# Kernel optimization log

Hardware: AMD Instinct MI355X
Metric: run time of the kernel (lower is better)

Reference implementation:

```python
import jax, jax.numpy as jnp
import numpy as np

TAU_CONVERGE = 0.01
N_STABLE = 2
B, L, DIM = 8, 4096, 1024
H, M = 16, 64
D_HEAD = DIM // H


def setup_inputs() -> dict:
    key = jax.random.key(0)
    k1, k2, k3, k4, k5, k6 = jax.random.split(key, 6)
    z_current = jax.random.normal(k1, (B, L, DIM), dtype=jnp.float32)
    # small perturbation so per-head velocity straddles tau_converge
    z_prev = z_current + 0.00125 * jax.random.normal(k2, (B, L, DIM), dtype=jnp.float32)
    codebook = jax.random.normal(k3, (H, M, D_HEAD), dtype=jnp.float32) * 0.02
    frozen_values = jax.random.normal(k4, (B, L, H, D_HEAD), dtype=jnp.float32)
    consecutive_converged = jax.random.randint(k5, (B, L, H), 0, 2, dtype=jnp.int32)
    crystallised = jax.random.randint(k6, (B, L, H), 0, 2) > 0
    return {
        "z_current": z_current,
        "z_prev": z_prev,
        "codebook": codebook,
        "frozen_values": frozen_values,
        "consecutive_converged": consecutive_converged,
        "crystallised": crystallised,
    }


def reference(z_current, z_prev, codebook, frozen_values, consecutive_converged, crystallised):
    """One crystallisation step: velocity -> counters -> snap-to-codebook -> enforce.

    Mirrors ConvergenceMonitor.update_and_crystallise followed by enforce(),
    with MultiHeadedCodebook.quantise(hard=True) for the codebook snap.
    All freeze/snap logic is outside the gradient graph (torch.no_grad/detach).
    """
    sg = jax.lax.stop_gradient
    zc = z_current.reshape(B, L, H, D_HEAD)   # [B,L,H,d]
    zp = z_prev.reshape(B, L, H, D_HEAD)

    # per-head velocity norm (detached in original)
    velocity = jnp.linalg.norm(sg(zc) - sg(zp), axis=-1)       # [B,L,H]
    converged = velocity < TAU_CONVERGE
    cc_new = jnp.where(converged, consecutive_converged + 1, 0)
    newly = (cc_new >= N_STABLE) & (~crystallised)             # [B,L,H] bool

    # hard nearest-neighbour quantise per head (no_grad in original)
    z_sg = sg(zc)
    cb = sg(codebook)
    # squared L2 distance: ||z||^2 - 2 z.c + ||c||^2  -> [B,L,H,M]
    d2 = (jnp.sum(z_sg * z_sg, axis=-1, keepdims=True)
          - 2.0 * jnp.einsum('blhd,hmd->blhm', z_sg, cb)
          + jnp.sum(cb * cb, axis=-1)[None, None])
    idx = jnp.argmin(d2, axis=-1)                              # [B,L,H]
    # gather nearest entries per head: codebook[h, idx[b,l,h]] -> [B,L,H,d]
    entries = cb[jnp.arange(H)[None, None, :], idx]

    # masked scatter of newly crystallised heads into frozen values
    frozen_new = jnp.where(newly[..., None], entries, sg(frozen_values))
    crystal_new = crystallised | newly

    # enforce: overwrite crystallised heads with frozen codebook values
    z_enforced = jnp.where(crystal_new[..., None], frozen_new, zc).reshape(B, L, DIM)
    return z_enforced, crystal_new, newly, cc_new, frozen_new
```

## Files before the change

### kernel.cpp

```cpp
#include <hip/hip_runtime.h>

#define BB 8
#define LL 4096
#define DIM 1024
#define HH 16
#define MM 64
#define DH 64

constexpr long long NZ = (long long)BB * LL * DIM;
constexpr long long NG = (long long)BB * LL * HH;
constexpr long long O_Z   = 0;
constexpr long long O_CRY = NZ;
constexpr long long O_NEW = NZ + NG;
constexpr long long O_CC  = NZ + 2 * NG;
constexpr long long O_FR  = NZ + 3 * NG;


#define ROWS 8

__global__ __launch_bounds__(256) void crystal_main(
    const float4* __restrict__ zc4,
    const float4* __restrict__ zp4,
    const float4* __restrict__ fr4,
    const int*    __restrict__ ccount,
    const int*    __restrict__ cryst,
    unsigned int* __restrict__ masks,
    float* __restrict__ out)
{
    __shared__ float lds_cry[ROWS * HH];
    __shared__ float lds_new[ROWS * HH];
    __shared__ float lds_cc [ROWS * HH];

    const int t   = threadIdx.x;
    const int h   = t >> 4;
    const int sub = t & 15;

    const long long row0 = (long long)blockIdx.x * ROWS;
    long long idx = row0 * (DIM / 4) + t;
    long long g   = row0 * HH + h;

    float4 zc = zc4[idx];
    float4 zp = zp4[idx];
    float4 fr = fr4[idx];
    int    cc = ccount[g];
    int    cv = cryst[g];

    unsigned int wmask = 0u;

    #pragma unroll
    for (int r = 0; r < ROWS; ++r) {
        const long long nidx = idx + (DIM / 4);
        const long long gn   = g + HH;
        float4 zcn, zpn, frn; int ccn_ = 0, cvn = 0;
        if (r < ROWS - 1) {
            zcn = zc4[nidx]; zpn = zp4[nidx]; frn = fr4[nidx];
            ccn_ = ccount[gn]; cvn = cryst[gn];
        }

        double s;
        {
            double dx = (double)zc.x - (double)zp.x;
            double dy = (double)zc.y - (double)zp.y;
            double dz = (double)zc.z - (double)zp.z;
            double dw = (double)zc.w - (double)zp.w;
            s = dx * dx + dy * dy + dz * dz + dw * dw;
        }
        s += __shfl_xor(s, 1);
        s += __shfl_xor(s, 2);
        s += __shfl_xor(s, 4);
        s += __shfl_xor(s, 8);

        const bool conv = sqrt(s) < 0.01;
        const int  ccn  = conv ? cc + 1 : 0;
        const bool cry  = cv != 0;
        const bool newly   = (ccn >= 2) && !cry;
        const bool crystal = cry || newly;

        float4 zout;
        zout.x = crystal ? fr.x : zc.x;
        zout.y = crystal ? fr.y : zc.y;
        zout.z = crystal ? fr.z : zc.z;
        zout.w = crystal ? fr.w : zc.w;

        reinterpret_cast<float4*>(out + O_Z)[idx]  = zout;
        reinterpret_cast<float4*>(out + O_FR)[idx] = fr;

        if (sub == 0) {
            lds_cry[r * HH + h] = crystal ? 1.0f : 0.0f;
            lds_new[r * HH + h] = newly   ? 1.0f : 0.0f;
            lds_cc [r * HH + h] = (float)ccn;
        }

        const unsigned long long bal = __ballot(newly && sub == 0);
        const unsigned int b4 = (unsigned int)((bal        & 1ull)       |
                                               ((bal >> 16) & 1ull) << 1 |
                                               ((bal >> 32) & 1ull) << 2 |
                                               ((bal >> 48) & 1ull) << 3);
        wmask |= b4 << (4 * r);

        zc = zcn; zp = zpn; fr = frn; cc = ccn_; cv = cvn;
        idx = nidx; g = gn;
    }

    if ((t & 63) == 0)
        masks[blockIdx.x * 4 + (t >> 6)] = wmask;

    __syncthreads();
    if (t < ROWS * HH) {
        const long long g0 = (long long)blockIdx.x * (ROWS * HH) + t;
        out[O_CRY + g0] = lds_cry[t];
        out[O_NEW + g0] = lds_new[t];
        out[O_CC  + g0] = lds_cc [t];
    }
}

#define MB_PER_CHUNK 4
#define CHUNK_ROWS  (MB_PER_CHUNK * ROWS)
#define NCHUNKS     (BB * LL / CHUNK_ROWS)

__global__ __launch_bounds__(64) void crystal_snap(
    const float4* __restrict__ zc4,
    const float*  __restrict__ cb,
    const unsigned int* __restrict__ masks,
    float* __restrict__ out)
{
    const int lane = threadIdx.x;
    const int h    = blockIdx.x / NCHUNKS;
    const int c    = blockIdx.x % NCHUNKS;
    const int w    = h >> 2;
    const int h2   = h & 3;

    const int mb = c * MB_PER_CHUNK + lane;
    const unsigned int word = (lane < MB_PER_CHUNK) ? masks[mb * 4 + w] : 0u;
    unsigned int rows8 = 0u;
    #pragma unroll
    for (int r = 0; r < ROWS; ++r)
        rows8 |= ((word >> (4 * r + h2)) & 1u) << r;

    unsigned long long act = __ballot(rows8 != 0u);
    if (act == 0ull) return;

    const float* cbh = cb + (long long)h * MM * DH;
    float4 crow[16];
    {
        const float4* cp = reinterpret_cast<const float4*>(cbh + lane * DH);
        #pragma unroll
        for (int k = 0; k < 16; ++k) crow[k] = cp[k];
    }

    int curl = 0; unsigned int curm8 = 0u;
    auto next_bl = [&]() -> long long {
        while (curm8 == 0u) {
            if (act == 0ull) return -1;
            curl = __ffsll(act) - 1; act &= act - 1;
            curm8 = __shfl(rows8, curl);
        }
        const int r = __ffs(curm8) - 1; curm8 &= curm8 - 1;
        return (long long)(c * MB_PER_CHUNK + curl) * ROWS + r;
    };

    long long bl = next_bl();
    long long seg4 = bl * (DIM / 4) + h * (DH / 4);
    float4 zv;
    if (lane < 16) zv = zc4[seg4 + lane];

    while (bl >= 0) {
        const long long bln = next_bl();
        const long long seg4n = bln * (DIM / 4) + h * (DH / 4);
        float4 zvn;
        if (bln >= 0 && lane < 16) zvn = zc4[seg4n + lane];

        double d2 = 0.0;
        #pragma unroll
        for (int k = 0; k < 16; ++k) {
            float4 zk;
            zk.x = __shfl(zv.x, k);
            zk.y = __shfl(zv.y, k);
            zk.z = __shfl(zv.z, k);
            zk.w = __shfl(zv.w, k);
            double a  = (double)zk.x - (double)crow[k].x;
            double b  = (double)zk.y - (double)crow[k].y;
            double cq = (double)zk.z - (double)crow[k].z;
            double d  = (double)zk.w - (double)crow[k].w;
            d2 += a * a + b * b + cq * cq + d * d;
        }

        double best = d2;
        int bidx = lane;
        #pragma unroll
        for (int m2 = 1; m2 <= 32; m2 <<= 1) {
            double ob = __shfl_xor(best, m2);
            int    oi = __shfl_xor(bidx, m2);
            if (ob < best || (ob == best && oi < bidx)) { best = ob; bidx = oi; }
        }

        if (lane < 16) {
            const float4 ev = reinterpret_cast<const float4*>(cbh + bidx * DH)[lane];
            reinterpret_cast<float4*>(out + O_Z)[seg4 + lane]  = ev;
            reinterpret_cast<float4*>(out + O_FR)[seg4 + lane] = ev;
        }

        bl = bln; seg4 = seg4n; zv = zvn;
    }
}

extern "C" void kernel_launch(void* const* d_in, const int* in_sizes, int n_in,
                              void* d_out, int out_size, void* d_ws, size_t ws_size,
                              hipStream_t stream) {
    const float4* zc4 = (const float4*)d_in[0];
    const float4* zp4 = (const float4*)d_in[1];
    const float*  cb  = (const float*)d_in[2];
    const float4* fr4 = (const float4*)d_in[3];
    const int*    cc  = (const int*)d_in[4];
    const int*    cry = (const int*)d_in[5];
    float* out = (float*)d_out;
    unsigned int* masks = (unsigned int*)d_ws;

    hipLaunchKernelGGL(crystal_main, dim3((BB * LL) / ROWS), dim3(256), 0, stream,
                       zc4, zp4, fr4, cc, cry, masks, out);
    hipLaunchKernelGGL(crystal_snap, dim3(HH * NCHUNKS), dim3(64), 0, stream,
                       zc4, cb, masks, out);
}
```

Measured before the change: 233.0 us.

## Fuse codebook snap into main kernel and skip redundant writes for newly heads

Merges the separate snap kernel into the main streaming kernel. Each wave handles its own newly-crystallised heads right after the row loop, so the mask workspace round-trip and the second launch go away. Heads that are newly crystallised no longer write z and frozen values in the main pass, since the snap pass overwrites them. The cost is that codebook rows are now loaded from memory per snap item instead of being held in registers, and snap work is serialised inside each block's tail.

```diff
diff --git a/kernel.cpp b/kernel.cpp
--- a/kernel.cpp
+++ b/kernel.cpp
@@ -18,22 +18,24 @@
 
 #define ROWS 8
 
-__global__ __launch_bounds__(256) void crystal_main(
+__global__ __launch_bounds__(256) void crystal_fused(
     const float4* __restrict__ zc4,
     const float4* __restrict__ zp4,
+    const float*  __restrict__ cb,
     const float4* __restrict__ fr4,
     const int*    __restrict__ ccount,
     const int*    __restrict__ cryst,
-    unsigned int* __restrict__ masks,
     float* __restrict__ out)
 {
     __shared__ float lds_cry[ROWS * HH];
     __shared__ float lds_new[ROWS * HH];
     __shared__ float lds_cc [ROWS * HH];
 
-    const int t   = threadIdx.x;
-    const int h   = t >> 4;
-    const int sub = t & 15;
+    const int t    = threadIdx.x;
+    const int h    = t >> 4;
+    const int sub  = t & 15;
+    const int lane = t & 63;
+    const int wv   = t >> 6;
 
     const long long row0 = (long long)blockIdx.x * ROWS;
     long long idx = row0 * (DIM / 4) + t;
@@ -76,14 +78,15 @@
         const bool newly   = (ccn >= 2) && !cry;
         const bool crystal = cry || newly;
 
-        float4 zout;
-        zout.x = crystal ? fr.x : zc.x;
-        zout.y = crystal ? fr.y : zc.y;
-        zout.z = crystal ? fr.z : zc.z;
-        zout.w = crystal ? fr.w : zc.w;
-
-        reinterpret_cast<float4*>(out + O_Z)[idx]  = zout;
-        reinterpret_cast<float4*>(out + O_FR)[idx] = fr;
+        if (!newly) {
+            float4 zout;
+            zout.x = crystal ? fr.x : zc.x;
+            zout.y = crystal ? fr.y : zc.y;
+            zout.z = crystal ? fr.z : zc.z;
+            zout.w = crystal ? fr.w : zc.w;
+            reinterpret_cast<float4*>(out + O_Z)[idx]  = zout;
+            reinterpret_cast<float4*>(out + O_FR)[idx] = fr;
+        }
 
         if (sub == 0) {
             lds_cry[r * HH + h] = crystal ? 1.0f : 0.0f;
@@ -102,75 +105,20 @@
         idx = nidx; g = gn;
     }
 
-    if ((t & 63) == 0)
-        masks[blockIdx.x * 4 + (t >> 6)] = wmask;
+    unsigned int items = wmask;
+    while (items) {
+        const int bit = __ffs(items) - 1; items &= items - 1;
+        const int r   = bit >> 2;
+        const int hh  = (wv << 2) | (bit & 3);
+        const long long bl   = row0 + r;
+        const long long seg4 = bl * (DIM / 4) + hh * (DH / 4);
+        const float* cbh = cb + (long long)hh * MM * DH;
 
-    __syncthreads();
-    if (t < ROWS * HH) {
-        const long long g0 = (long long)blockIdx.x * (ROWS * HH) + t;
-        out[O_CRY + g0] = lds_cry[t];
-        out[O_NEW + g0] = lds_new[t];
-        out[O_CC  + g0] = lds_cc [t];
-    }
-}
-
-#define MB_PER_CHUNK 4
-#define CHUNK_ROWS  (MB_PER_CHUNK * ROWS)
-#define NCHUNKS     (BB * LL / CHUNK_ROWS)
-
-__global__ __launch_bounds__(64) void crystal_snap(
-    const float4* __restrict__ zc4,
-    const float*  __restrict__ cb,
-    const unsigned int* __restrict__ masks,
-    float* __restrict__ out)
-{
-    const int lane = threadIdx.x;
-    const int h    = blockIdx.x / NCHUNKS;
-    const int c    = blockIdx.x % NCHUNKS;
-    const int w    = h >> 2;
-    const int h2   = h & 3;
-
-    const int mb = c * MB_PER_CHUNK + lane;
-    const unsigned int word = (lane < MB_PER_CHUNK) ? masks[mb * 4 + w] : 0u;
-    unsigned int rows8 = 0u;
-    #pragma unroll
-    for (int r = 0; r < ROWS; ++r)
-        rows8 |= ((word >> (4 * r + h2)) & 1u) << r;
-
-    unsigned long long act = __ballot(rows8 != 0u);
-    if (act == 0ull) return;
-
-    const float* cbh = cb + (long long)h * MM * DH;
-    float4 crow[16];
-    {
-        const float4* cp = reinterpret_cast<const float4*>(cbh + lane * DH);
-        #pragma unroll
-        for (int k = 0; k < 16; ++k) crow[k] = cp[k];
-    }
-
-    int curl = 0; unsigned int curm8 = 0u;
-    auto next_bl = [&]() -> long long {
-        while (curm8 == 0u) {
-            if (act == 0ull) return -1;
-            curl = __ffsll(act) - 1; act &= act - 1;
-            curm8 = __shfl(rows8, curl);
-        }
-        const int r = __ffs(curm8) - 1; curm8 &= curm8 - 1;
-        return (long long)(c * MB_PER_CHUNK + curl) * ROWS + r;
-    };
-
-    long long bl = next_bl();
-    long long seg4 = bl * (DIM / 4) + h * (DH / 4);
-    float4 zv;
-    if (lane < 16) zv = zc4[seg4 + lane];
-
-    while (bl >= 0) {
-        const long long bln = next_bl();
-        const long long seg4n = bln * (DIM / 4) + h * (DH / 4);
-        float4 zvn;
-        if (bln >= 0 && lane < 16) zvn = zc4[seg4n + lane];
+        float4 zv;
+        if (lane < 16) zv = zc4[seg4 + lane];
 
         double d2 = 0.0;
+        const float4* crow = reinterpret_cast<const float4*>(cbh + lane * DH);
         #pragma unroll
         for (int k = 0; k < 16; ++k) {
             float4 zk;
@@ -178,10 +126,11 @@
             zk.y = __shfl(zv.y, k);
             zk.z = __shfl(zv.z, k);
             zk.w = __shfl(zv.w, k);
-            double a  = (double)zk.x - (double)crow[k].x;
-            double b  = (double)zk.y - (double)crow[k].y;
-            double cq = (double)zk.z - (double)crow[k].z;
-            double d  = (double)zk.w - (double)crow[k].w;
+            const float4 cvv = crow[k];
+            double a  = (double)zk.x - (double)cvv.x;
+            double b  = (double)zk.y - (double)cvv.y;
+            double cq = (double)zk.z - (double)cvv.z;
+            double d  = (double)zk.w - (double)cvv.w;
             d2 += a * a + b * b + cq * cq + d * d;
         }
 
@@ -199,8 +148,14 @@
             reinterpret_cast<float4*>(out + O_Z)[seg4 + lane]  = ev;
             reinterpret_cast<float4*>(out + O_FR)[seg4 + lane] = ev;
         }
+    }
 
-        bl = bln; seg4 = seg4n; zv = zvn;
+    __syncthreads();
+    if (t < ROWS * HH) {
+        const long long g0 = (long long)blockIdx.x * (ROWS * HH) + t;
+        out[O_CRY + g0] = lds_cry[t];
+        out[O_NEW + g0] = lds_new[t];
+        out[O_CC  + g0] = lds_cc [t];
     }
 }
 
@@ -214,10 +169,7 @@
     const int*    cc  = (const int*)d_in[4];
     const int*    cry = (const int*)d_in[5];
     float* out = (float*)d_out;
-    unsigned int* masks = (unsigned int*)d_ws;
 
-    hipLaunchKernelGGL(crystal_main, dim3((BB * LL) / ROWS), dim3(256), 0, stream,
-                       zc4, zp4, fr4, cc, cry, masks, out);
-    hipLaunchKernelGGL(crystal_snap, dim3(HH * NCHUNKS), dim3(64), 0, stream,
-                       zc4, cb, masks, out);
+    hipLaunchKernelGGL(crystal_fused, dim3((BB * LL) / ROWS), dim3(256), 0, stream,
+                       zc4, zp4, cb, fr4, cc, cry, out);
 }
```

After: 346.1 us. 1.49x slower.
